# Kernel tuning notes

Measured on AMD Instinct MI355X. Metric: run time of the kernel, lower is better.

The kernel has to match this reference:

```python
import jax, jax.numpy as jnp
import numpy as np

EPS = 1e-12

def _l2norm(v):
    # torch.nn.functional.normalize(p=2) with eps clamp
    return v / jnp.maximum(jnp.linalg.norm(v), EPS)

def _spectral_weight(W, U):
    # W: (out, in) flattened 1x1 conv weight; U: (1, out) power-iteration buffer.
    # One power iteration, all under stop_gradient (torch.no_grad in original).
    V = _l2norm(U @ W)            # (1, in)
    Unew = _l2norm(V @ W.T)       # (1, out)
    sigma = (Unew @ W @ V.T)[0, 0]
    return W / jax.lax.stop_gradient(sigma)

def _conv1x1(x, W, b):
    # x: (b,c,h,w), W: (o,c), b: (o,)
    return jnp.einsum('oc,bchw->bohw', W, x) + b[None, :, None, None]

def setup_inputs() -> dict:
    key = jax.random.key(0)
    ks = jax.random.split(key, 11)
    B, C, H, W = 4, 256, 64, 64
    Ck = C // 8
    return {
        'x':   jax.random.normal(ks[0], (B, C, H, W), jnp.float32),
        'f_w': jax.random.normal(ks[1], (Ck, C), jnp.float32) * 0.05,
        'f_b': jax.random.normal(ks[2], (Ck,), jnp.float32) * 0.05,
        'f_u': jax.random.uniform(ks[3], (1, Ck), jnp.float32),
        'g_w': jax.random.normal(ks[4], (Ck, C), jnp.float32) * 0.05,
        'g_b': jax.random.normal(ks[5], (Ck,), jnp.float32) * 0.05,
        'g_u': jax.random.uniform(ks[6], (1, Ck), jnp.float32),
        'h_w': jax.random.normal(ks[7], (C, C), jnp.float32) * 0.05,
        'h_b': jax.random.normal(ks[8], (C,), jnp.float32) * 0.05,
        'h_u': jax.random.uniform(ks[9], (1, C), jnp.float32),
        'gamma': jax.random.normal(ks[10], (1, 1), jnp.float32),
    }

def reference(x, f_w, f_b, f_u, g_w, g_b, g_u, h_w, h_b, h_u, gamma):
    b, c, h, w = x.shape
    hw = h * w
    key_ = _conv1x1(x, _spectral_weight(f_w, f_u), f_b).reshape(b, -1, hw).transpose(0, 2, 1)  # (b,hw,ck)
    query = _conv1x1(x, _spectral_weight(g_w, g_u), g_b).reshape(b, -1, hw)                    # (b,ck,hw)
    attn = jax.nn.softmax(jnp.einsum('bnd,bdm->bnm', key_, query), axis=-1)                    # (b,hw,hw)
    value = _conv1x1(x, _spectral_weight(h_w, h_u), h_b).reshape(b, -1, hw)                    # (b,c,hw)
    out = jnp.einsum('bnm,bcm->bnc', attn, value)                                              # (b,hw,c)
    # Faithful to original: raw view of (b,hw,c) contiguous buffer into (b,c,h,w)
    out = out.reshape(b, c, h, w)
    return gamma[0, 0] * out + x
```

## Files before the change

kernel.cpp:

```cpp
#include <hip/hip_runtime.h>


constexpr int kC   = 256;
constexpr int kHW  = 4096;
constexpr int kB   = 4;
constexpr int kCHW = kC * kHW;

typedef short bf16x8 __attribute__((ext_vector_type(8)));
typedef float f32x4  __attribute__((ext_vector_type(4)));
typedef unsigned short u16;

#if __has_builtin(__builtin_amdgcn_exp2f)
#define EXP2(x) __builtin_amdgcn_exp2f(x)
#else
#define EXP2(x) exp2f(x)
#endif

__device__ __forceinline__ u16 f2bf(float f) {
    union { float f; unsigned u; } v; v.f = f;
    unsigned u = v.u;
    return (u16)((u + 0x7fffu + ((u >> 16) & 1u)) >> 16);
}
__device__ __forceinline__ float bf2f(u16 h) {
    union { unsigned u; float f; } v; v.u = ((unsigned)h) << 16;
    return v.f;
}

__global__ __launch_bounds__(1024) void k_prep(
    const float* __restrict__ fw, const float* __restrict__ fu,
    const float* __restrict__ gw, const float* __restrict__ gu,
    const float* __restrict__ hww, const float* __restrict__ hu,
    float* __restrict__ sig, u16* __restrict__ wh, u16* __restrict__ wl)
{
    if (blockIdx.x >= 3) {
        const int tid = (blockIdx.x - 3) * 1024 + threadIdx.x;
        const int g  = tid >> 8;
        const int ci = tid & 255;
        const float f = (g < 32) ? fw[g * 256 + ci]
                      : (g < 64) ? gw[(g - 32) * 256 + ci]
                                 : hww[(g - 64) * 256 + ci];
        const int idx = ((g >> 4) * 8 + (ci >> 5)) * 512 + (g & 15) * 32 + (ci & 31);
        const u16 h = f2bf(f);
        wh[idx] = h;
        wl[idx] = f2bf(f - bf2f(h));
        return;
    }

    const int which = blockIdx.x;
    const float* W = which == 0 ? fw : (which == 1 ? gw : hww);
    const float* U = which == 0 ? fu : (which == 1 ? gu : hu);
    const int O = (which == 2) ? 256 : 32;
    const int t = threadIdx.x;

    __shared__ float par[4][256];
    __shared__ float red[256];
    __shared__ __align__(16) float Vv[256];

    {
        const int i = t & 255, och = t >> 8;
        float p = 0.f;
        if (O == 256) {
            const float* Wc = W + (size_t)(och * 64) * 256 + i;
            const float* Uc = U + och * 64;
#pragma unroll 8
            for (int oo = 0; oo < 64; ++oo)
                p += Uc[oo] * Wc[(size_t)oo * 256];
        } else if (och == 0) {
            const float* Wc = W + i;
#pragma unroll 8
            for (int oo = 0; oo < 32; ++oo)
                p += U[oo] * Wc[(size_t)oo * 256];
        }
        par[och][i] = p;
    }
    __syncthreads();
    float t1 = 0.f;
    if (t < 256) {
        t1 = par[0][t] + par[1][t] + par[2][t] + par[3][t];
        red[t] = t1 * t1;
    }
    __syncthreads();
    for (int s = 128; s > 0; s >>= 1) { if (t < s) red[t] += red[t + s]; __syncthreads(); }
    if (t < 256) Vv[t] = t1 / fmaxf(sqrtf(red[0]), 1e-12f);
    __syncthreads();

    {
        const int o = t & 255, ich = t >> 8;
        float q = 0.f;
        if (o < O) {
            const float4* Wr = (const float4*)(W + (size_t)o * 256 + ich * 64);
            const float4* Vr = (const float4*)(&Vv[ich * 64]);
#pragma unroll
            for (int j = 0; j < 16; ++j) {
                const float4 w = Wr[j]; const float4 v = Vr[j];
                q += w.x * v.x + w.y * v.y + w.z * v.z + w.w * v.w;
            }
        }
        par[ich][o] = q;
    }
    __syncthreads();
    if (t < 256) {
        const float t2 = par[0][t] + par[1][t] + par[2][t] + par[3][t];
        red[t] = t2 * t2;
    }
    __syncthreads();
    for (int s = 128; s > 0; s >>= 1) { if (t < s) red[t] += red[t + s]; __syncthreads(); }
    if (t == 0) {
        const float s2 = red[0];
        sig[which] = fmaxf(sqrtf(s2), 1e-12f) / s2;
    }
}

__global__ __launch_bounds__(512) void k_proj(
    const float* __restrict__ x,
    const u16* __restrict__ wh, const u16* __restrict__ wl,
    const float* __restrict__ fb, const float* __restrict__ gb,
    const float* __restrict__ hb, const float* __restrict__ sig,
    u16* __restrict__ Kc, u16* __restrict__ Qc, u16* __restrict__ Vb)
{
    __shared__ __align__(16) float xs[256][64];
    __shared__ float bLDS[320];

    const int t = threadIdx.x;
    const int wave = t >> 6, lane = t & 63;
    const int quad = lane >> 4, l15 = lane & 15;
    const int b = blockIdx.y;
    const int n0 = blockIdx.x * 64;
    const int nch = wave & 3, cohalf = wave >> 2;

    constexpr float kLog2e = 1.44269504f;

    {
        const int r4i = lane >> 4, c16 = lane & 15;
        const float* xg = x + (size_t)b * kCHW + (size_t)r4i * kHW + n0 + c16 * 4;
#pragma unroll
        for (int j = 0; j < 8; ++j) {
            const int cibase = (wave * 8 + j) * 4;
            __builtin_amdgcn_global_load_lds(
                (const __attribute__((address_space(1))) void*)(xg + (size_t)cibase * kHW),
                (__attribute__((address_space(3))) void*)&xs[cibase][0], 16, 0, 0);
        }
    }
    if (t < 320) bLDS[t] = (t < 32) ? fb[t]
                         : (t < 64) ? gb[t - 32] * kLog2e
                         : hb[t - 64];
    __syncthreads();

    const int n = nch * 16 + l15;
    bf16x8 bh[8], bl[8];
#pragma unroll
    for (int s = 0; s < 8; ++s) {
        union { u16 a[8]; bf16x8 v; } H, L;
#pragma unroll
        for (int j = 0; j < 8; ++j) {
            const float v = xs[s * 32 + quad * 8 + j][n];
            const u16 h = f2bf(v);
            H.a[j] = h; L.a[j] = f2bf(v - bf2f(h));
        }
        bh[s] = H.v; bl[s] = L.v;
    }

    const u16* whp = wh + l15 * 32 + quad * 8;
    const u16* wlp = wl + l15 * 32 + quad * 8;

    f32x4 acc[10] = {};
#pragma unroll
    for (int c = 0; c < 10; ++c) {
        const size_t base = (size_t)(cohalf * 10 + c) * 4096;
#pragma unroll
        for (int s = 0; s < 8; ++s) {
            const bf16x8 ah = *(const bf16x8*)(whp + base + s * 512);
            const bf16x8 al = *(const bf16x8*)(wlp + base + s * 512);
            acc[c] = __builtin_amdgcn_mfma_f32_16x16x32_bf16(ah, bh[s], acc[c], 0, 0, 0);
            acc[c] = __builtin_amdgcn_mfma_f32_16x16x32_bf16(ah, bl[s], acc[c], 0, 0, 0);
            acc[c] = __builtin_amdgcn_mfma_f32_16x16x32_bf16(al, bh[s], acc[c], 0, 0, 0);
        }
    }

    const float s0 = sig[0], s1 = sig[1] * kLog2e, s2 = sig[2];
#pragma unroll
    for (int c = 0; c < 10; ++c) {
        const int cog0 = (cohalf * 10 + c) * 16;
        const float inv = (cog0 < 32) ? s0 : (cog0 < 64) ? s1 : s2;
        if (cog0 < 64) {
            u16 hi[4], lo[4];
#pragma unroll
            for (int r = 0; r < 4; ++r) {
                const float v = acc[c][r] * inv + bLDS[cog0 + quad * 4 + r];
                hi[r] = f2bf(v);
                lo[r] = f2bf(v - bf2f(hi[r]));
            }
            u16* H = (cog0 < 32) ? Kc : Qc;
            const int dbase = (cog0 & 31) + quad * 4;
            const size_t off = (size_t)(b * kHW + n0 + n) * 64;
            const unsigned h01 = (unsigned)hi[0] | ((unsigned)hi[1] << 16);
            const unsigned h23 = (unsigned)hi[2] | ((unsigned)hi[3] << 16);
            const unsigned l01 = (unsigned)lo[0] | ((unsigned)lo[1] << 16);
            const unsigned l23 = (unsigned)lo[2] | ((unsigned)lo[3] << 16);
            *(uint2*)(H + off + dbase)      = make_uint2(h01, h23);
            *(uint2*)(H + off + 32 + dbase) = make_uint2(l01, l23);
        } else {
#pragma unroll
            for (int r = 0; r < 4; ++r) {
                const int co = cog0 + quad * 4 + r;
                const float v = acc[c][r] * inv + bLDS[co];
                Vb[((size_t)b * kC + (co - 64)) * kHW + n0 + n] = f2bf(v);
            }
        }
    }
}

__global__ __launch_bounds__(512, 4) void k_attn(
    const u16* __restrict__ Kc, const u16* __restrict__ Qc,
    const u16* __restrict__ Vb,
    u16* __restrict__ Op, float* __restrict__ Sl)
{
    __shared__ __align__(16) u16 Qt[2][4096];
    __shared__ __align__(16) u16 Pt[2][4096];
    __shared__ float lsum[8][16];

    const int t = threadIdx.x;
    const int wave = t >> 6, lane = t & 63;
    const int quad = lane >> 4, l15 = lane & 15;
    const int sg = wave >> 1, half = wave & 1;

    const int id = blockIdx.x;
    const int xcd = id & 7;
    const int b = xcd >> 1;
    const int nb0 = ((xcd & 1) * 32 + ((id >> 3) & 31)) * 64;
    const int mh = id >> 8;
    const int mt0 = mh * 32, mt1 = mt0 + 32;

    const u16* Kb  = Kc + (size_t)b * kHW * 64;
    const u16* Qb  = Qc + (size_t)b * kHW * 64;
    const u16* Vbb = Vb + (size_t)b * kC * kHW;

    const size_t krow = (size_t)(nb0 + sg * 16 + l15) * 64 + (size_t)quad * 8;
    const bf16x8 kh = *(const bf16x8*)(Kb + krow);
    const bf16x8 kl = *(const bf16x8*)(Kb + krow + 32);

    const u16* vrow[2];
#pragma unroll
    for (int ct = 0; ct < 2; ++ct)
        vrow[ct] = Vbb + (size_t)(wave * 32 + ct * 16 + l15) * kHW + quad * 8;

    const int qs_row = lane >> 3, qs_ch = lane & 7;
    const int rloc = wave * 8 + qs_row;
    const int qswz = (qs_ch ^ (rloc & 7)) << 3;

    f32x4 O[8] = {};
    float lrow = 0.f;
    bf16x8 vc[4];

    __builtin_amdgcn_global_load_lds(
        (const __attribute__((address_space(1))) void*)
            (Qb + (size_t)(mt0 * 64 + rloc) * 64 + qswz),
        (__attribute__((address_space(3))) void*)&Qt[0][wave * 512], 16, 0, 0);
    __syncthreads();

    for (int mt = mt0; mt < mt1; ++mt) {
        const int cur = mt & 1;
        const int m0 = mt * 64;

        if (mt < mt1 - 1) {
            __builtin_amdgcn_global_load_lds(
                (const __attribute__((address_space(1))) void*)
                    (Qb + (size_t)(m0 + 64 + rloc) * 64 + qswz),
                (__attribute__((address_space(3))) void*)&Qt[cur ^ 1][wave * 512], 16, 0, 0);
        }
#pragma unroll
        for (int ct = 0; ct < 2; ++ct)
#pragma unroll
            for (int ks = 0; ks < 2; ++ks)
                vc[ct * 2 + ks] = *(const bf16x8*)(vrow[ct] + m0 + ks * 32);

        f32x4 s[2];
        __builtin_amdgcn_s_setprio(1);
#pragma unroll
        for (int mi2 = 0; mi2 < 2; ++mi2) {
            const int mi = half * 2 + mi2;
            const int rbase = (mi * 16 + l15) * 64;
            const bf16x8 qhv = *(const bf16x8*)&Qt[cur][rbase + ((quad       ^ (l15 & 7)) << 3)];
            const bf16x8 qlv = *(const bf16x8*)&Qt[cur][rbase + (((quad + 4) ^ (l15 & 7)) << 3)];
            f32x4 a = { 0.f, 0.f, 0.f, 0.f };
            a = __builtin_amdgcn_mfma_f32_16x16x32_bf16(qhv, kl, a, 0, 0, 0);
            a = __builtin_amdgcn_mfma_f32_16x16x32_bf16(qlv, kh, a, 0, 0, 0);
            a = __builtin_amdgcn_mfma_f32_16x16x32_bf16(qhv, kh, a, 0, 0, 0);
            s[mi2] = a;
        }
        __builtin_amdgcn_s_setprio(0);

        {
            const int prow = sg * 16 + l15;
#pragma unroll
            for (int mi2 = 0; mi2 < 2; ++mi2) {
                const float p0 = EXP2(s[mi2][0]);
                const float p1 = EXP2(s[mi2][1]);
                const float p2 = EXP2(s[mi2][2]);
                const float p3 = EXP2(s[mi2][3]);
                lrow += (p0 + p1) + (p2 + p3);
                const unsigned d0 = __builtin_amdgcn_perm(
                    __float_as_uint(p1), __float_as_uint(p0), 0x07060302u);
                const unsigned d1 = __builtin_amdgcn_perm(
                    __float_as_uint(p3), __float_as_uint(p2), 0x07060302u);
                const int mi = half * 2 + mi2;
                const int chunk = 2 * mi + (quad >> 1);
                const int off = prow * 64 + ((chunk ^ (l15 & 7)) << 3) + (quad & 1) * 4;
                *(uint2*)(Pt[cur] + off) = make_uint2(d0, d1);
            }
        }

        __syncthreads();

        __builtin_amdgcn_s_setprio(1);
#pragma unroll
        for (int ks = 0; ks < 2; ++ks) {
#pragma unroll
            for (int rg = 0; rg < 4; ++rg) {
                const bf16x8 pa = *(const bf16x8*)&Pt[cur][(rg * 16 + l15) * 64
                                     + (((ks * 4 + quad) ^ (l15 & 7)) << 3)];
#pragma unroll
                for (int ct = 0; ct < 2; ++ct)
                    O[rg * 2 + ct] = __builtin_amdgcn_mfma_f32_16x16x32_bf16(
                        pa, vc[ct * 2 + ks], O[rg * 2 + ct], 0, 0, 0);
            }
        }
        __builtin_amdgcn_s_setprio(0);
    }

    lrow += __shfl_xor(lrow, 16);
    lrow += __shfl_xor(lrow, 32);
    if (lane < 16) lsum[wave][l15] = lrow;
    __syncthreads();
    if (half == 0 && lane < 16)
        Sl[(size_t)(mh * 4 + b) * kHW + nb0 + sg * 16 + l15]
            = lsum[wave][l15] + lsum[wave ^ 1][l15];

    u16* Opb = Op + (size_t)(mh * 4 + b) * kHW * 256;
#pragma unroll
    for (int rg = 0; rg < 4; ++rg) {
#pragma unroll
        for (int ct = 0; ct < 2; ++ct) {
#pragma unroll
            for (int r = 0; r < 4; ++r) {
                const int nn = nb0 + rg * 16 + quad * 4 + r;
                const int c = wave * 32 + ct * 16 + l15;
                Opb[(size_t)nn * 256 + c] = f2bf(O[rg * 2 + ct][r]);
            }
        }
    }
}

__global__ __launch_bounds__(256) void k_merge(
    const float* __restrict__ x, const float* __restrict__ gamma,
    const u16* __restrict__ Op, const float* __restrict__ Sl,
    float* __restrict__ out)
{
    const int tid = blockIdx.x * 256 + threadIdx.x;
    const int cg = tid & 31;
    const int n  = (tid >> 5) & 4095;
    const int b  = tid >> 17;
    const int c0 = cg * 8;

    const float la = Sl[(size_t)b * kHW + n];
    const float lb = Sl[(size_t)(4 + b) * kHW + n];
    const float invL = 1.f / (la + lb);
    const float g = gamma[0];

    const size_t base = ((size_t)b * kHW + n) * 256 + c0;
    const uint4 A = *(const uint4*)(Op + base);
    const uint4 B = *(const uint4*)(Op + base + (size_t)4 * kHW * 256);
    const float4 x0 = *(const float4*)(x + base);
    const float4 x1 = *(const float4*)(x + base + 4);

    float o[8];
    const unsigned aw[4] = { A.x, A.y, A.z, A.w };
    const unsigned bw[4] = { B.x, B.y, B.z, B.w };
#pragma unroll
    for (int j = 0; j < 8; ++j) {
        const float va = bf2f((u16)(aw[j >> 1] >> ((j & 1) * 16)));
        const float vb = bf2f((u16)(bw[j >> 1] >> ((j & 1) * 16)));
        o[j] = (va + vb) * invL;
    }
    float4 r0, r1;
    r0.x = g * o[0] + x0.x; r0.y = g * o[1] + x0.y;
    r0.z = g * o[2] + x0.z; r0.w = g * o[3] + x0.w;
    r1.x = g * o[4] + x1.x; r1.y = g * o[5] + x1.y;
    r1.z = g * o[6] + x1.z; r1.w = g * o[7] + x1.w;
    *(float4*)(out + base)     = r0;
    *(float4*)(out + base + 4) = r1;
}

extern "C" void kernel_launch(void* const* d_in, const int* in_sizes, int n_in,
                              void* d_out, int out_size, void* d_ws, size_t ws_size,
                              hipStream_t stream)
{
    const float* x     = (const float*)d_in[0];
    const float* fw    = (const float*)d_in[1];
    const float* fb    = (const float*)d_in[2];
    const float* fu    = (const float*)d_in[3];
    const float* gw    = (const float*)d_in[4];
    const float* gb    = (const float*)d_in[5];
    const float* gu    = (const float*)d_in[6];
    const float* hww   = (const float*)d_in[7];
    const float* hb    = (const float*)d_in[8];
    const float* hu    = (const float*)d_in[9];
    const float* gamma = (const float*)d_in[10];
    float* out = (float*)d_out;

    char* ws = (char*)d_ws;
    float* sig = (float*)ws;
    u16* wh = (u16*)(ws + 1024);
    u16* wl = wh + 320 * 256;
    u16* Kc = (u16*)(ws + (1u << 20));
    u16* Qc = (u16*)(ws + (3u << 20));
    u16* Vb = (u16*)(ws + (5u << 20));
    u16* Op = (u16*)(ws + (16u << 20));
    float* Sl = (float*)(ws + (32u << 20));

    k_prep<<<dim3(83), dim3(1024), 0, stream>>>(fw, fu, gw, gu, hww, hu, sig, wh, wl);
    k_proj<<<dim3(64, 4), dim3(512), 0, stream>>>(x, wh, wl, fb, gb, hb, sig,
                                                  Kc, Qc, Vb);
    k_attn<<<dim3(512), dim3(512), 0, stream>>>(Kc, Qc, Vb, Op, Sl);
    k_merge<<<dim3(2048), dim3(256), 0, stream>>>(x, gamma, Op, Sl, out);
}
```

Measured before the change: 216.2 us.

## Keep softmax probabilities in registers and retile V for direct MFMA PV

The attention kernel permutes which Q rows each lane computes, so the exp'd score MFMA output can be reused directly as the A operand of the PV MFMA. This removes the LDS staging buffer for P and the LDS reads that went with it. To make this work, V is written by the projection kernel in a tiled layout, and each wave now accumulates all 256 channels for its 16 rows over half of each key tile. That produces four partial outputs that a templated merge kernel sums. In exchange, accumulator registers double, V global loads per wave grow, and the extra partial output buffers add write and read traffic.

```diff
diff --git a/kernel.cpp b/kernel.cpp
--- a/kernel.cpp
+++ b/kernel.cpp
@@ -178,6 +178,8 @@
     }
 
     const float s0 = sig[0], s1 = sig[1] * kLog2e, s2 = sig[2];
+    const int m = n0 + n;
+    const size_t vmbase = (size_t)b * kC * kHW + ((size_t)(m >> 5) * 256) * 32 + (m & 31);
 #pragma unroll
     for (int c = 0; c < 10; ++c) {
         const int cog0 = (cohalf * 10 + c) * 16;
@@ -192,7 +194,7 @@
             }
             u16* H = (cog0 < 32) ? Kc : Qc;
             const int dbase = (cog0 & 31) + quad * 4;
-            const size_t off = (size_t)(b * kHW + n0 + n) * 64;
+            const size_t off = (size_t)(b * kHW + m) * 64;
             const unsigned h01 = (unsigned)hi[0] | ((unsigned)hi[1] << 16);
             const unsigned h23 = (unsigned)hi[2] | ((unsigned)hi[3] << 16);
             const unsigned l01 = (unsigned)lo[0] | ((unsigned)lo[1] << 16);
@@ -204,7 +206,7 @@
             for (int r = 0; r < 4; ++r) {
                 const int co = cog0 + quad * 4 + r;
                 const float v = acc[c][r] * inv + bLDS[co];
-                Vb[((size_t)b * kC + (co - 64)) * kHW + n0 + n] = f2bf(v);
+                Vb[vmbase + (size_t)(co - 64) * 32] = f2bf(v);
             }
         }
     }
@@ -216,7 +218,6 @@
     u16* __restrict__ Op, float* __restrict__ Sl)
 {
     __shared__ __align__(16) u16 Qt[2][4096];
-    __shared__ __align__(16) u16 Pt[2][4096];
     __shared__ float lsum[8][16];
 
     const int t = threadIdx.x;
@@ -239,18 +240,14 @@
     const bf16x8 kh = *(const bf16x8*)(Kb + krow);
     const bf16x8 kl = *(const bf16x8*)(Kb + krow + 32);
 
-    const u16* vrow[2];
-#pragma unroll
-    for (int ct = 0; ct < 2; ++ct)
-        vrow[ct] = Vbb + (size_t)(wave * 32 + ct * 16 + l15) * kHW + quad * 8;
-
     const int qs_row = lane >> 3, qs_ch = lane & 7;
     const int rloc = wave * 8 + qs_row;
     const int qswz = (qs_ch ^ (rloc & 7)) << 3;
 
-    f32x4 O[8] = {};
+    const int rho0 = half * 32 + ((l15 >> 2) << 3) + (l15 & 3);
+
+    f32x4 O[16] = {};
     float lrow = 0.f;
-    bf16x8 vc[4];
 
     __builtin_amdgcn_global_load_lds(
         (const __attribute__((address_space(1))) void*)
@@ -268,20 +265,15 @@
                     (Qb + (size_t)(m0 + 64 + rloc) * 64 + qswz),
                 (__attribute__((address_space(3))) void*)&Qt[cur ^ 1][wave * 512], 16, 0, 0);
         }
-#pragma unroll
-        for (int ct = 0; ct < 2; ++ct)
-#pragma unroll
-            for (int ks = 0; ks < 2; ++ks)
-                vc[ct * 2 + ks] = *(const bf16x8*)(vrow[ct] + m0 + ks * 32);
 
         f32x4 s[2];
         __builtin_amdgcn_s_setprio(1);
 #pragma unroll
         for (int mi2 = 0; mi2 < 2; ++mi2) {
-            const int mi = half * 2 + mi2;
-            const int rbase = (mi * 16 + l15) * 64;
-            const bf16x8 qhv = *(const bf16x8*)&Qt[cur][rbase + ((quad       ^ (l15 & 7)) << 3)];
-            const bf16x8 qlv = *(const bf16x8*)&Qt[cur][rbase + (((quad + 4) ^ (l15 & 7)) << 3)];
+            const int rho = rho0 + mi2 * 4;
+            const int rsw = rho & 7;
+            const bf16x8 qhv = *(const bf16x8*)&Qt[cur][rho * 64 + ((quad       ^ rsw) << 3)];
+            const bf16x8 qlv = *(const bf16x8*)&Qt[cur][rho * 64 + (((quad + 4) ^ rsw) << 3)];
             f32x4 a = { 0.f, 0.f, 0.f, 0.f };
             a = __builtin_amdgcn_mfma_f32_16x16x32_bf16(qhv, kl, a, 0, 0, 0);
             a = __builtin_amdgcn_mfma_f32_16x16x32_bf16(qlv, kh, a, 0, 0, 0);
@@ -290,42 +282,31 @@
         }
         __builtin_amdgcn_s_setprio(0);
 
+        union { unsigned u[4]; bf16x8 v; } PA;
         {
-            const int prow = sg * 16 + l15;
-#pragma unroll
-            for (int mi2 = 0; mi2 < 2; ++mi2) {
-                const float p0 = EXP2(s[mi2][0]);
-                const float p1 = EXP2(s[mi2][1]);
-                const float p2 = EXP2(s[mi2][2]);
-                const float p3 = EXP2(s[mi2][3]);
-                lrow += (p0 + p1) + (p2 + p3);
-                const unsigned d0 = __builtin_amdgcn_perm(
-                    __float_as_uint(p1), __float_as_uint(p0), 0x07060302u);
-                const unsigned d1 = __builtin_amdgcn_perm(
-                    __float_as_uint(p3), __float_as_uint(p2), 0x07060302u);
-                const int mi = half * 2 + mi2;
-                const int chunk = 2 * mi + (quad >> 1);
-                const int off = prow * 64 + ((chunk ^ (l15 & 7)) << 3) + (quad & 1) * 4;
-                *(uint2*)(Pt[cur] + off) = make_uint2(d0, d1);
+            const float e00 = EXP2(s[0][0]), e01 = EXP2(s[0][1]);
+            const float e02 = EXP2(s[0][2]), e03 = EXP2(s[0][3]);
+            const float e10 = EXP2(s[1][0]), e11 = EXP2(s[1][1]);
+            const float e12 = EXP2(s[1][2]), e13 = EXP2(s[1][3]);
+            lrow += ((e00 + e01) + (e02 + e03)) + ((e10 + e11) + (e12 + e13));
+            PA.u[0] = __builtin_amdgcn_perm(__float_as_uint(e01), __float_as_uint(e00), 0x07060302u);
+            PA.u[1] = __builtin_amdgcn_perm(__float_as_uint(e03), __float_as_uint(e02), 0x07060302u);
+            PA.u[2] = __builtin_amdgcn_perm(__float_as_uint(e11), __float_as_uint(e10), 0x07060302u);
+            PA.u[3] = __builtin_amdgcn_perm(__float_as_uint(e13), __float_as_uint(e12), 0x07060302u);
+        }
+
+        {
+            const u16* vb = Vbb + (size_t)(mt * 2 + half) * 8192 + l15 * 32 + quad * 8;
+            __builtin_amdgcn_s_setprio(1);
+#pragma unroll
+            for (int ct = 0; ct < 16; ++ct) {
+                const bf16x8 vv = *(const bf16x8*)(vb + ct * 512);
+                O[ct] = __builtin_amdgcn_mfma_f32_16x16x32_bf16(PA.v, vv, O[ct], 0, 0, 0);
             }
+            __builtin_amdgcn_s_setprio(0);
         }
 
         __syncthreads();
-
-        __builtin_amdgcn_s_setprio(1);
-#pragma unroll
-        for (int ks = 0; ks < 2; ++ks) {
-#pragma unroll
-            for (int rg = 0; rg < 4; ++rg) {
-                const bf16x8 pa = *(const bf16x8*)&Pt[cur][(rg * 16 + l15) * 64
-                                     + (((ks * 4 + quad) ^ (l15 & 7)) << 3)];
-#pragma unroll
-                for (int ct = 0; ct < 2; ++ct)
-                    O[rg * 2 + ct] = __builtin_amdgcn_mfma_f32_16x16x32_bf16(
-                        pa, vc[ct * 2 + ks], O[rg * 2 + ct], 0, 0, 0);
-            }
-        }
-        __builtin_amdgcn_s_setprio(0);
     }
 
     lrow += __shfl_xor(lrow, 16);
@@ -336,21 +317,19 @@
         Sl[(size_t)(mh * 4 + b) * kHW + nb0 + sg * 16 + l15]
             = lsum[wave][l15] + lsum[wave ^ 1][l15];
 
-    u16* Opb = Op + (size_t)(mh * 4 + b) * kHW * 256;
-#pragma unroll
-    for (int rg = 0; rg < 4; ++rg) {
-#pragma unroll
-        for (int ct = 0; ct < 2; ++ct) {
-#pragma unroll
-            for (int r = 0; r < 4; ++r) {
-                const int nn = nb0 + rg * 16 + quad * 4 + r;
-                const int c = wave * 32 + ct * 16 + l15;
-                Opb[(size_t)nn * 256 + c] = f2bf(O[rg * 2 + ct][r]);
-            }
-        }
-    }
-}
-
+    u16* Opb = Op + ((size_t)(mh * 2 + half) * 4 + b) * (size_t)kHW * 256;
+#pragma unroll
+    for (int ct = 0; ct < 16; ++ct) {
+#pragma unroll
+        for (int r = 0; r < 4; ++r) {
+            const int nn = nb0 + sg * 16 + quad * 4 + r;
+            const int c = ct * 16 + l15;
+            Opb[(size_t)nn * 256 + c] = f2bf(O[ct][r]);
+        }
+    }
+}
+
+template <int NS>
 __global__ __launch_bounds__(256) void k_merge(
     const float* __restrict__ x, const float* __restrict__ gamma,
     const u16* __restrict__ Op, const float* __restrict__ Sl,
@@ -368,25 +347,24 @@
     const float g = gamma[0];
 
     const size_t base = ((size_t)b * kHW + n) * 256 + c0;
-    const uint4 A = *(const uint4*)(Op + base);
-    const uint4 B = *(const uint4*)(Op + base + (size_t)4 * kHW * 256);
+
+    float o[8] = {};
+#pragma unroll
+    for (int s = 0; s < NS; ++s) {
+        const uint4 A = *(const uint4*)(Op + base + (size_t)s * 4 * kHW * 256);
+        const unsigned aw[4] = { A.x, A.y, A.z, A.w };
+#pragma unroll
+        for (int j = 0; j < 8; ++j)
+            o[j] += bf2f((u16)(aw[j >> 1] >> ((j & 1) * 16)));
+    }
+
     const float4 x0 = *(const float4*)(x + base);
     const float4 x1 = *(const float4*)(x + base + 4);
-
-    float o[8];
-    const unsigned aw[4] = { A.x, A.y, A.z, A.w };
-    const unsigned bw[4] = { B.x, B.y, B.z, B.w };
-#pragma unroll
-    for (int j = 0; j < 8; ++j) {
-        const float va = bf2f((u16)(aw[j >> 1] >> ((j & 1) * 16)));
-        const float vb = bf2f((u16)(bw[j >> 1] >> ((j & 1) * 16)));
-        o[j] = (va + vb) * invL;
-    }
     float4 r0, r1;
-    r0.x = g * o[0] + x0.x; r0.y = g * o[1] + x0.y;
-    r0.z = g * o[2] + x0.z; r0.w = g * o[3] + x0.w;
-    r1.x = g * o[4] + x1.x; r1.y = g * o[5] + x1.y;
-    r1.z = g * o[6] + x1.z; r1.w = g * o[7] + x1.w;
+    r0.x = g * o[0] * invL + x0.x; r0.y = g * o[1] * invL + x0.y;
+    r0.z = g * o[2] * invL + x0.z; r0.w = g * o[3] * invL + x0.w;
+    r1.x = g * o[4] * invL + x1.x; r1.y = g * o[5] * invL + x1.y;
+    r1.z = g * o[6] * invL + x1.z; r1.w = g * o[7] * invL + x1.w;
     *(float4*)(out + base)     = r0;
     *(float4*)(out + base + 4) = r1;
 }
@@ -412,15 +390,15 @@
     float* sig = (float*)ws;
     u16* wh = (u16*)(ws + 1024);
     u16* wl = wh + 320 * 256;
-    u16* Kc = (u16*)(ws + (1u << 20));
-    u16* Qc = (u16*)(ws + (3u << 20));
-    u16* Vb = (u16*)(ws + (5u << 20));
-    u16* Op = (u16*)(ws + (16u << 20));
-    float* Sl = (float*)(ws + (32u << 20));
+    u16* Kc = (u16*)(ws + (512u << 10));
+    u16* Qc = (u16*)(ws + (2560u << 10));
+    u16* Vb = (u16*)(ws + (4608u << 10));
+    u16* Op = (u16*)(ws + (12800u << 10));
+    float* Sl = (float*)(ws + (12800u << 10) + 4ull * 8 * 1024 * 1024);
 
     k_prep<<<dim3(83), dim3(1024), 0, stream>>>(fw, fu, gw, gu, hww, hu, sig, wh, wl);
     k_proj<<<dim3(64, 4), dim3(512), 0, stream>>>(x, wh, wl, fb, gb, hb, sig,
                                                   Kc, Qc, Vb);
     k_attn<<<dim3(512), dim3(512), 0, stream>>>(Kc, Qc, Vb, Op, Sl);
-    k_merge<<<dim3(2048), dim3(256), 0, stream>>>(x, gamma, Op, Sl, out);
-}
+    k_merge<4><<<dim3(2048), dim3(256), 0, stream>>>(x, gamma, Op, Sl, out);
+}
```

Result: slower. 269.4 us (+24.6%).
